# Kernel tuning notes

Hardware: AMD Instinct MI355X
Metric: run time of the kernel (lower is better)

## Reference

```python
import jax, jax.numpy as jnp
import numpy as np

B, S, H, V, T, L = 32, 128, 1024, 32000, 50, 3


def _ln(x, g, b, eps=1e-5):
    m = x.mean(-1, keepdims=True)
    v = ((x - m) ** 2).mean(-1, keepdims=True)
    return (x - m) / jnp.sqrt(v + eps) * g + b


def setup_inputs() -> dict:
    key = jax.random.key(0)
    ks = iter(jax.random.split(key, 48))
    r = lambda shape, s=0.02: jax.random.normal(next(ks), shape, jnp.float32) * s
    return dict(
        encoder_outputs=jax.random.normal(next(ks), (B, S, H), jnp.float32),
        h0=jax.random.normal(next(ks), (L, B, H), jnp.float32),
        c0=jax.random.normal(next(ks), (L, B, H), jnp.float32),
        valid_src_len=jax.random.randint(next(ks), (B,), 1, S + 1),
        target=jax.random.randint(next(ks), (B, T), 0, V),
        embedding=r((V, H), 1.0),
        Wa=r((H, H)), ba=jnp.zeros((H,)),
        Ua=r((H, H)), ub=jnp.zeros((H,)),
        Va=r((1, H)), vb=jnp.zeros((1,)),
        temperature=jnp.ones((1,)),
        Wih0=r((4 * H, 2 * H)), Whh0=r((4 * H, H)), bih0=jnp.zeros((4 * H,)), bhh0=jnp.zeros((4 * H,)),
        Wih1=r((4 * H, H)), Whh1=r((4 * H, H)), bih1=jnp.zeros((4 * H,)), bhh1=jnp.zeros((4 * H,)),
        Wih2=r((4 * H, H)), Whh2=r((4 * H, H)), bih2=jnp.zeros((4 * H,)), bhh2=jnp.zeros((4 * H,)),
        fc_w=r((V, H)), fc_b=jnp.zeros((V,)),
        eng=jnp.ones((H,)), enb=jnp.zeros((H,)),
        cng=jnp.ones((H,)), cnb=jnp.zeros((H,)),
        ong=jnp.ones((H,)), onb=jnp.zeros((H,)),
    )


def _decode(encoder_outputs, h0, c0, valid_src_len, target, p):
    mask = jnp.arange(S)[None, :] < valid_src_len[:, None]           # (B,S)
    Ukeys = encoder_outputs @ p['Ua'].T + p['ub']                    # (B,S,H) precomputed Ua(keys)
    Wih = (p['Wih0'], p['Wih1'], p['Wih2'])
    Whh = (p['Whh0'], p['Whh1'], p['Whh2'])
    bih = (p['bih0'], p['bih1'], p['bih2'])
    bhh = (p['bhh0'], p['bhh1'], p['bhh2'])
    # teacher forcing: token at step t is start_token (0) for t=0, else target[:, t-1]
    tokens = jnp.concatenate([jnp.zeros((B, 1), target.dtype), target[:, :-1]], 1).T  # (T,B)

    def step(carry, tok):
        h, c = carry                                                 # each (L,B,H)
        emb = _ln(p['embedding'][tok], p['eng'], p['enb'])           # (B,H); dropout omitted (eval)
        q = h[-1]                                                    # (B,H) query = top-layer h
        s = jnp.tanh((q @ p['Wa'].T + p['ba'])[:, None, :] + Ukeys)  # (B,S,H)
        scores = (jnp.einsum('bsh,h->bs', s, p['Va'][0]) + p['vb'][0]) / p['temperature'][0]
        scores = jnp.where(mask, scores, -1e9)
        w = jax.nn.softmax(scores, axis=-1)                          # (B,S)
        ctx = _ln(jnp.einsum('bs,bsh->bh', w, encoder_outputs), p['cng'], p['cnb'])
        x = jnp.concatenate([emb, ctx], axis=-1)                     # (B,2H)
        hs, cs = [], []
        for l in range(L):                                           # 3 stacked LSTM layers
            g = x @ Wih[l].T + bih[l] + h[l] @ Whh[l].T + bhh[l]
            i_, f_, g_, o_ = jnp.split(g, 4, axis=-1)                # torch gate order i,f,g,o
            cl = jax.nn.sigmoid(f_) * c[l] + jax.nn.sigmoid(i_) * jnp.tanh(g_)
            hl = jax.nn.sigmoid(o_) * jnp.tanh(cl)
            hs.append(hl); cs.append(cl); x = hl
        out = _ln(x, p['ong'], p['onb'])
        logits = out @ p['fc_w'].T + p['fc_b']                       # (B,V)
        return (jnp.stack(hs), jnp.stack(cs)), (logits, w)

    (hT, cT), (logits, attn) = jax.lax.scan(step, (h0, c0), tokens)
    return logits.transpose(1, 0, 2), hT, cT, attn.transpose(1, 0, 2)


def reference(encoder_outputs, h0, c0, valid_src_len, target, embedding, Wa, ba, Ua, ub, Va, vb,
              temperature, Wih0, Whh0, bih0, bhh0, Wih1, Whh1, bih1, bhh1, Wih2, Whh2, bih2, bhh2,
              fc_w, fc_b, eng, enb, cng, cnb, ong, onb):
    p = dict(embedding=embedding, Wa=Wa, ba=ba, Ua=Ua, ub=ub, Va=Va, vb=vb, temperature=temperature,
             Wih0=Wih0, Whh0=Whh0, bih0=bih0, bhh0=bhh0, Wih1=Wih1, Whh1=Whh1, bih1=bih1, bhh1=bhh1,
             Wih2=Wih2, Whh2=Whh2, bih2=bih2, bhh2=bhh2, fc_w=fc_w, fc_b=fc_b,
             eng=eng, enb=enb, cng=cng, cnb=cnb, ong=ong, onb=onb)
    logits, hT, cT, attn = _decode(encoder_outputs, h0, c0, valid_src_len, target, p)
    return logits, (hT, cT), attn
```

## Files before the change

kernel.cpp:

```cpp
#include <hip/hip_runtime.h>
#include <math.h>

#define DEV_INLINE __device__ __forceinline__

constexpr int B = 32, S = 128, H = 1024, V = 32000, T = 50, L = 3;
constexpr int H2 = 2 * H, H4 = 4 * H;
constexpr int BH = B * H;
constexpr int MTOT = T * B;

constexpr size_t HT_OFF   = (size_t)B * T * V;
constexpr size_t CT_OFF   = HT_OFF + (size_t)L * B * H;
constexpr size_t ATTN_OFF = CT_OFF + (size_t)L * B * H;

constexpr size_t WS_UKEYS = 0;
constexpr size_t WS_EMBBF = WS_UKEYS + (size_t)B * S * H;
constexpr size_t WS_H2ALL = WS_EMBBF + (size_t)T * BH / 2;
constexpr size_t WS_H     = WS_H2ALL + (size_t)T * BH;
constexpr size_t WS_C     = WS_H + (size_t)L * BH;
constexpr size_t WS_QWA   = WS_C + (size_t)L * BH;
constexpr size_t WS_SCO   = WS_QWA + (size_t)BH;
constexpr size_t WS_GAT   = WS_SCO + (size_t)B * S;
constexpr size_t WS_HBF   = WS_GAT + (size_t)B * H4;
constexpr size_t WS_XCBF  = WS_HBF + (size_t)2 * L * BH / 2;
constexpr size_t WS_OLALL = WS_XCBF + (size_t)B * H2 / 2;
constexpr size_t WS_WBF   = WS_OLALL + (size_t)T * BH / 2;

constexpr size_t OW_WA   = 0;
constexpr size_t OW_WIH0 = OW_WA   + (size_t)H * H;
constexpr size_t OW_WHH0 = OW_WIH0 + (size_t)H4 * H2;
constexpr size_t OW_WIH1 = OW_WHH0 + (size_t)H4 * H;
constexpr size_t OW_WHH1 = OW_WIH1 + (size_t)H4 * H;
constexpr size_t OW_WIH2 = OW_WHH1 + (size_t)H4 * H;
constexpr size_t OW_WHH2 = OW_WIH2 + (size_t)H4 * H;
constexpr size_t OW_FCW  = OW_WHH2 + (size_t)H4 * H;
constexpr size_t OW_END  = OW_FCW  + (size_t)V * H;
constexpr size_t NEED_WS_BYTES = WS_WBF * 4 + OW_END * 2;

typedef __attribute__((ext_vector_type(8))) short short8;
typedef __attribute__((ext_vector_type(4))) float f32x4;
typedef __attribute__((ext_vector_type(4))) unsigned short u16x4;

DEV_INLINE float sigmoidf_(float x) { return 1.f / (1.f + expf(-x)); }

DEV_INLINE unsigned short bf16u(float f) {
  union { float f; unsigned u; } v; v.f = f;
  unsigned r = v.u + 0x7fffu + ((v.u >> 16) & 1u);
  return (unsigned short)(r >> 16);
}

DEV_INLINE float wave_sum(float v) {
#pragma unroll
  for (int o = 32; o; o >>= 1) v += __shfl_xor(v, o, 64);
  return v;
}

DEV_INLINE float blk_sum256(float v, float* buf) {
  v = wave_sum(v);
  __syncthreads();
  if ((threadIdx.x & 63) == 0) buf[threadIdx.x >> 6] = v;
  __syncthreads();
  return buf[0] + buf[1] + buf[2] + buf[3];
}

__global__ void k_init(const float* __restrict__ h0, const float* __restrict__ c0,
                       float* __restrict__ hst, float* __restrict__ cst,
                       unsigned short* __restrict__ hbf) {
  int idx = blockIdx.x * 256 + threadIdx.x;
  if (idx < L * BH) { hst[idx] = h0[idx]; hbf[idx] = bf16u(h0[idx]); }
  else cst[idx - L * BH] = c0[idx - L * BH];
}

__global__ void k_fin(const float* __restrict__ hst, const float* __restrict__ h2src,
                      const float* __restrict__ cst, float* __restrict__ out) {
  int idx = blockIdx.x * 256 + threadIdx.x;
  if (idx < 2 * BH) out[HT_OFF + idx] = hst[idx];
  else if (idx < 3 * BH) out[HT_OFF + idx] = h2src[idx - 2 * BH];
  else out[HT_OFF + idx] = cst[idx - 3 * BH];
}

constexpr int NCVT = 8;
struct CvtArgs { const float* src[NCVT]; unsigned short* dst[NCVT]; };
constexpr int CV_N4[NCVT] = {
  H * H / 4, H4 * H2 / 4, H4 * H / 4, H4 * H / 4, H4 * H / 4,
  H4 * H / 4, H4 * H / 4, V * H / 4};
__global__ void k_cvt_all(CvtArgs a) {
  int cum[NCVT + 1]; cum[0] = 0;
#pragma unroll
  for (int r = 0; r < NCVT; ++r) cum[r + 1] = cum[r] + CV_N4[r];
  const int total = cum[NCVT];
  int i = blockIdx.x * 256 + threadIdx.x;
  const int stride = gridDim.x * 256;
  for (; i < total; i += stride) {
    int r = 0;
#pragma unroll
    for (int q = 0; q < NCVT; ++q) r += (i >= cum[q + 1]) ? 1 : 0;
    int off = i - cum[r];
    f32x4 v = *(const f32x4*)(a.src[r] + (size_t)off * 4);
    u16x4 o;
    o[0] = bf16u(v[0]); o[1] = bf16u(v[1]); o[2] = bf16u(v[2]); o[3] = bf16u(v[3]);
    *(u16x4*)(a.dst[r] + (size_t)off * 4) = o;
  }
}

__global__ __launch_bounds__(512) void k_ukeys_mfma(
    const float* __restrict__ X, const float* __restrict__ W,
    const float* __restrict__ bias, float* __restrict__ C) {
  __shared__ unsigned short As[128][72];
  __shared__ unsigned short Bs[128][72];
  const int tid = threadIdx.x, lane = tid & 63, wid = tid >> 6;
  const int wm = wid >> 2, wn = wid & 3;
  const int n0 = blockIdx.x * 128, m0 = blockIdx.y * 128;
  const int fr = lane & 15, kg = lane >> 4;
  f32x4 acc[4][2];
#pragma unroll
  for (int i = 0; i < 4; ++i)
#pragma unroll
    for (int j = 0; j < 2; ++j) acc[i][j] = {0.f, 0.f, 0.f, 0.f};
  for (int k0 = 0; k0 < H; k0 += 64) {
    __syncthreads();
#pragma unroll
    for (int r = 0; r < 4; ++r) {
      int i = tid + 512 * r;
      int row = i >> 4, c4 = (i & 15) * 4;
      f32x4 v = *(const f32x4*)(X + (size_t)(m0 + row) * H + k0 + c4);
      u16x4 o;
      o[0] = bf16u(v[0]); o[1] = bf16u(v[1]); o[2] = bf16u(v[2]); o[3] = bf16u(v[3]);
      *(u16x4*)&As[row][c4] = o;
    }
#pragma unroll
    for (int r = 0; r < 4; ++r) {
      int i = tid + 512 * r;
      int row = i >> 4, c4 = (i & 15) * 4;
      f32x4 v = *(const f32x4*)(W + (size_t)(n0 + row) * H + k0 + c4);
      u16x4 o;
      o[0] = bf16u(v[0]); o[1] = bf16u(v[1]); o[2] = bf16u(v[2]); o[3] = bf16u(v[3]);
      *(u16x4*)&Bs[row][c4] = o;
    }
    __syncthreads();
#pragma unroll
    for (int kk = 0; kk < 64; kk += 32) {
      short8 av[4], bv[2];
#pragma unroll
      for (int fm = 0; fm < 4; ++fm)
        av[fm] = *(const short8*)&As[wm * 64 + fm * 16 + fr][kk + kg * 8];
#pragma unroll
      for (int fn = 0; fn < 2; ++fn)
        bv[fn] = *(const short8*)&Bs[wn * 32 + fn * 16 + fr][kk + kg * 8];
#pragma unroll
      for (int fm = 0; fm < 4; ++fm)
#pragma unroll
        for (int fn = 0; fn < 2; ++fn)
          acc[fm][fn] = __builtin_amdgcn_mfma_f32_16x16x32_bf16(av[fm], bv[fn],
                                                                acc[fm][fn], 0, 0, 0);
    }
  }
#pragma unroll
  for (int fm = 0; fm < 4; ++fm)
#pragma unroll
    for (int fn = 0; fn < 2; ++fn)
#pragma unroll
      for (int r = 0; r < 4; ++r) {
        int m = m0 + wm * 64 + fm * 16 + kg * 4 + r;
        int n = n0 + wn * 32 + fn * 16 + fr;
        C[(size_t)m * H + n] = acc[fm][fn][r] + bias[n];
      }
}

__global__ __launch_bounds__(256) void k_gemm_nt(
    const float* __restrict__ A, const float* __restrict__ Bw,
    const float* __restrict__ bias, float* __restrict__ C, int N, int K) {
  __shared__ float As[16][132];
  __shared__ float Bs[16][68];
  const int i0 = blockIdx.y * 128, j0 = blockIdx.x * 64;
  const int ty = threadIdx.x >> 4, tx = threadIdx.x & 15;
  float acc[8][4] = {};
  for (int k0 = 0; k0 < K; k0 += 16) {
#pragma unroll
    for (int r = 0; r < 8; ++r) {
      int i = threadIdx.x + 256 * r;
      int mm = i >> 4, kk = i & 15;
      As[kk][mm] = A[(size_t)(i0 + mm) * K + k0 + kk];
    }
#pragma unroll
    for (int r = 0; r < 4; ++r) {
      int i = threadIdx.x + 256 * r;
      int nn = i >> 4, kk = i & 15;
      Bs[kk][nn] = Bw[(size_t)(j0 + nn) * K + k0 + kk];
    }
    __syncthreads();
#pragma unroll
    for (int kk = 0; kk < 16; ++kk) {
      float a[8], bb[4];
#pragma unroll
      for (int i = 0; i < 8; ++i) a[i] = As[kk][ty * 8 + i];
#pragma unroll
      for (int j = 0; j < 4; ++j) bb[j] = Bs[kk][tx * 4 + j];
#pragma unroll
      for (int i = 0; i < 8; ++i)
#pragma unroll
        for (int j = 0; j < 4; ++j) acc[i][j] = fmaf(a[i], bb[j], acc[i][j]);
    }
    __syncthreads();
  }
#pragma unroll
  for (int i = 0; i < 8; ++i) {
    size_t row = (size_t)(i0 + ty * 8 + i) * N;
#pragma unroll
    for (int j = 0; j < 4; ++j) {
      int col = j0 + tx * 4 + j;
      C[row + col] = acc[i][j] + bias[col];
    }
  }
}

__global__ void k_embln(const float* __restrict__ table, const int* __restrict__ target,
                        const float* __restrict__ g, const float* __restrict__ bta,
                        unsigned short* __restrict__ out) {
  __shared__ float rbuf[4];
  int idx = blockIdx.x;
  int t = idx >> 5, b = idx & 31;
  int tok = (t == 0) ? 0 : target[b * T + (t - 1)];
  const float* e = table + (size_t)tok * H;
  int tid = threadIdx.x;
  float x[4];
#pragma unroll
  for (int r = 0; r < 4; ++r) x[r] = e[r * 256 + tid];
  float m = blk_sum256(x[0] + x[1] + x[2] + x[3], rbuf) * (1.f / H);
  float vs = 0.f;
#pragma unroll
  for (int r = 0; r < 4; ++r) { float d = x[r] - m; vs += d * d; }
  float var = blk_sum256(vs, rbuf) * (1.f / H);
  float rstd = rsqrtf(var + 1e-5f);
  unsigned short* o = out + (size_t)idx * H;
#pragma unroll
  for (int r = 0; r < 4; ++r) {
    int h = r * 256 + tid;
    o[h] = bf16u((x[r] - m) * rstd * g[h] + bta[h]);
  }
}

__global__ void k_scores(const float* __restrict__ qwa, const float* __restrict__ ukeys,
                         const float* __restrict__ va, const float* __restrict__ vb,
                         const float* __restrict__ temp, const int* __restrict__ vlen,
                         float* __restrict__ sco) {
  int lane = threadIdx.x & 63, wid = threadIdx.x >> 6;
  int idx = blockIdx.x * 4 + wid;
  int b = idx >> 7, s = idx & 127;
  const float* uk = ukeys + (size_t)idx * H;
  const float* q = qwa + (size_t)b * H;
  float a = 0.f;
#pragma unroll
  for (int i = 0; i < 16; ++i) {
    int k = i * 64 + lane;
    a = fmaf(va[k], tanhf(q[k] + uk[k]), a);
  }
  a = wave_sum(a);
  if (lane == 0) {
    float val = (a + vb[0]) / temp[0];
    if (s >= vlen[b]) val = -1e9f;
    sco[idx] = val;
  }
}

__global__ void k_smctx(const float* __restrict__ sco, const float* __restrict__ enc,
                        const unsigned short* __restrict__ embt, const float* __restrict__ g,
                        const float* __restrict__ bta, unsigned short* __restrict__ xbf,
                        float* __restrict__ attn, int t) {
  __shared__ float sw[S];
  __shared__ float rbuf[4];
  int b = blockIdx.x, tid = threadIdx.x;
  if (tid < 64) {
    float v0 = sco[b * S + tid], v1 = sco[b * S + 64 + tid];
    float m = fmaxf(v0, v1);
#pragma unroll
    for (int o = 32; o; o >>= 1) m = fmaxf(m, __shfl_xor(m, o, 64));
    float e0 = expf(v0 - m), e1 = expf(v1 - m);
    float ssum = wave_sum(e0 + e1);
    float inv = 1.f / ssum;
    sw[tid] = e0 * inv;
    sw[64 + tid] = e1 * inv;
  }
  __syncthreads();
  if (tid < S) attn[((size_t)b * T + t) * S + tid] = sw[tid];
  float v[4] = {0.f, 0.f, 0.f, 0.f};
  for (int s2 = 0; s2 < S; ++s2) {
    float wv = sw[s2];
    const float* er = enc + ((size_t)b * S + s2) * H;
#pragma unroll
    for (int r = 0; r < 4; ++r) v[r] = fmaf(wv, er[r * 256 + tid], v[r]);
  }
  float m = blk_sum256(v[0] + v[1] + v[2] + v[3], rbuf) * (1.f / H);
  float vs = 0.f;
#pragma unroll
  for (int r = 0; r < 4; ++r) { float d = v[r] - m; vs += d * d; }
  float var = blk_sum256(vs, rbuf) * (1.f / H);
  float rstd = rsqrtf(var + 1e-5f);
  unsigned short* xr = xbf + (size_t)b * H2;
#pragma unroll
  for (int r = 0; r < 4; ++r) {
    int h = r * 256 + tid;
    xr[H + h] = bf16u((v[r] - m) * rstd * g[h] + bta[h]);
    xr[h] = embt[(size_t)b * H + h];
  }
}

__global__ __launch_bounds__(256) void k_skinny_bf(
    const unsigned short* __restrict__ x, const unsigned short* __restrict__ Wb, int K,
    const float* __restrict__ bias, float* __restrict__ out, int obstride) {
  __shared__ float red[4][32][16];
  const int lane = threadIdx.x & 63, wid = threadIdx.x >> 6;
  const int jb = blockIdx.x * 16;
  const int jl = lane & 15, kg = lane >> 4;
  f32x4 acc0 = {0.f, 0.f, 0.f, 0.f}, acc1 = {0.f, 0.f, 0.f, 0.f};
  const int per = (K >> 5) >> 2;
  const int send = (wid + 1) * per;
  for (int s = wid * per; s < send; ++s) {
    const int ke = s * 32 + kg * 8;
    short8 bw = *(const short8*)(Wb + (size_t)(jb + jl) * K + ke);
    short8 a0 = *(const short8*)(x + (size_t)jl * K + ke);
    short8 a1 = *(const short8*)(x + (size_t)(16 + jl) * K + ke);
    acc0 = __builtin_amdgcn_mfma_f32_16x16x32_bf16(a0, bw, acc0, 0, 0, 0);
    acc1 = __builtin_amdgcn_mfma_f32_16x16x32_bf16(a1, bw, acc1, 0, 0, 0);
  }
#pragma unroll
  for (int r = 0; r < 4; ++r) {
    red[wid][kg * 4 + r][jl] = acc0[r];
    red[wid][16 + kg * 4 + r][jl] = acc1[r];
  }
  __syncthreads();
  const int tid = threadIdx.x;
#pragma unroll
  for (int u = 0; u < 2; ++u) {
    int oi = tid * 2 + u;
    int m = oi >> 4, j = oi & 15;
    float v = red[0][m][j] + red[1][m][j] + red[2][m][j] + red[3][m][j];
    int jg = jb + j;
    out[(size_t)m * obstride + jg] = v + bias[jg];
  }
}

__global__ __launch_bounds__(256) void k_gates4(
    const unsigned short* __restrict__ x1, int K1,
    const unsigned short* __restrict__ x2, int K2,
    const unsigned short* __restrict__ W1, const unsigned short* __restrict__ W2,
    const float* __restrict__ bih, const float* __restrict__ bhh,
    float* __restrict__ cl, float* __restrict__ hl, unsigned short* __restrict__ hbfw) {
  __shared__ float red[4][32][17];
  const int lane = threadIdx.x & 63, wid = threadIdx.x >> 6;
  const int jb = blockIdx.x * 4;
  const int fr = lane & 15, kg = lane >> 4;
  const int wrow = (fr >> 2) * H + jb + (fr & 3);
  f32x4 acc0 = {0.f, 0.f, 0.f, 0.f}, acc1 = {0.f, 0.f, 0.f, 0.f};
  const int s1 = K1 >> 5, s2 = K2 >> 5;
  const int per = (s1 + s2) >> 2;
  const int sbeg = wid * per, send = sbeg + per;
  const int e1 = send < s1 ? send : s1;
#pragma unroll 4
  for (int s = sbeg; s < e1; ++s) {
    const int ke = s * 32 + kg * 8;
    short8 bw = *(const short8*)(W1 + (size_t)wrow * K1 + ke);
    short8 a0 = *(const short8*)(x1 + (size_t)fr * K1 + ke);
    short8 a1 = *(const short8*)(x1 + (size_t)(16 + fr) * K1 + ke);
    acc0 = __builtin_amdgcn_mfma_f32_16x16x32_bf16(a0, bw, acc0, 0, 0, 0);
    acc1 = __builtin_amdgcn_mfma_f32_16x16x32_bf16(a1, bw, acc1, 0, 0, 0);
  }
  const int b2 = sbeg > s1 ? sbeg : s1;
#pragma unroll 4
  for (int s = b2; s < send; ++s) {
    const int ke = (s - s1) * 32 + kg * 8;
    short8 bw = *(const short8*)(W2 + (size_t)wrow * K2 + ke);
    short8 a0 = *(const short8*)(x2 + (size_t)fr * K2 + ke);
    short8 a1 = *(const short8*)(x2 + (size_t)(16 + fr) * K2 + ke);
    acc0 = __builtin_amdgcn_mfma_f32_16x16x32_bf16(a0, bw, acc0, 0, 0, 0);
    acc1 = __builtin_amdgcn_mfma_f32_16x16x32_bf16(a1, bw, acc1, 0, 0, 0);
  }
#pragma unroll
  for (int r = 0; r < 4; ++r) {
    red[wid][kg * 4 + r][fr] = acc0[r];
    red[wid][16 + kg * 4 + r][fr] = acc1[r];
  }
  __syncthreads();
  const int tid = threadIdx.x;
  if (tid < 128) {
    int m = tid >> 2, jj = tid & 3, kcol = jb + jj;
    float gate[4];
#pragma unroll
    for (int g = 0; g < 4; ++g) {
      int f = g * 4 + jj;
      gate[g] = red[0][m][f] + red[1][m][f] + red[2][m][f] + red[3][m][f]
              + bih[g * H + kcol] + bhh[g * H + kcol];
    }
    int idx = m * H + kcol;
    float cn = sigmoidf_(gate[1]) * cl[idx] + sigmoidf_(gate[0]) * tanhf(gate[2]);
    float hn = sigmoidf_(gate[3]) * tanhf(cn);
    cl[idx] = cn;
    hl[idx] = hn;
    hbfw[idx] = bf16u(hn);
  }
}

__global__ void k_ln_all(const float* __restrict__ h2all, const float* __restrict__ g,
                         const float* __restrict__ bta, unsigned short* __restrict__ olbf) {
  __shared__ float rbuf[4];
  int row = blockIdx.x, tid = threadIdx.x;
  const float* hr = h2all + (size_t)row * H;
  float hv[4];
#pragma unroll
  for (int r = 0; r < 4; ++r) hv[r] = hr[r * 256 + tid];
  float m = blk_sum256(hv[0] + hv[1] + hv[2] + hv[3], rbuf) * (1.f / H);
  float vs = 0.f;
#pragma unroll
  for (int r = 0; r < 4; ++r) { float d = hv[r] - m; vs += d * d; }
  float var = blk_sum256(vs, rbuf) * (1.f / H);
  float rstd = rsqrtf(var + 1e-5f);
  unsigned short* o = olbf + (size_t)row * H;
#pragma unroll
  for (int r = 0; r < 4; ++r) {
    int k = r * 256 + tid;
    o[k] = bf16u((hv[r] - m) * rstd * g[k] + bta[k]);
  }
}

__global__ __launch_bounds__(512) void k_logits(
    const unsigned short* __restrict__ X, const unsigned short* __restrict__ Wb,
    const float* __restrict__ bias, float* __restrict__ out) {
  __shared__ unsigned short As[128][72];
  __shared__ unsigned short Bs[128][72];
  const int tid = threadIdx.x, lane = tid & 63, wid = tid >> 6;
  const int wm = wid >> 2, wn = wid & 3;
  const int n0 = blockIdx.x * 128, m0 = blockIdx.y * 128;
  const int fr = lane & 15, kg = lane >> 4;
  f32x4 acc[4][2];
#pragma unroll
  for (int i = 0; i < 4; ++i)
#pragma unroll
    for (int j = 0; j < 2; ++j) acc[i][j] = {0.f, 0.f, 0.f, 0.f};
  const short8 zero8 = {0, 0, 0, 0, 0, 0, 0, 0};
  for (int k0 = 0; k0 < H; k0 += 64) {
    __syncthreads();
#pragma unroll
    for (int r = 0; r < 2; ++r) {
      int i = tid + 512 * r, row = i >> 3, c8 = (i & 7) * 8;
      int gm = m0 + row;
      short8 v = (gm < MTOT) ? *(const short8*)(X + (size_t)gm * H + k0 + c8) : zero8;
      *(short8*)&As[row][c8] = v;
    }
#pragma unroll
    for (int r = 0; r < 2; ++r) {
      int i = tid + 512 * r, row = i >> 3, c8 = (i & 7) * 8;
      *(short8*)&Bs[row][c8] = *(const short8*)(Wb + (size_t)(n0 + row) * H + k0 + c8);
    }
    __syncthreads();
#pragma unroll
    for (int kk = 0; kk < 64; kk += 32) {
      short8 av[4], bv[2];
#pragma unroll
      for (int fm = 0; fm < 4; ++fm)
        av[fm] = *(const short8*)&As[wm * 64 + fm * 16 + fr][kk + kg * 8];
#pragma unroll
      for (int fn = 0; fn < 2; ++fn)
        bv[fn] = *(const short8*)&Bs[wn * 32 + fn * 16 + fr][kk + kg * 8];
#pragma unroll
      for (int fm = 0; fm < 4; ++fm)
#pragma unroll
        for (int fn = 0; fn < 2; ++fn)
          acc[fm][fn] = __builtin_amdgcn_mfma_f32_16x16x32_bf16(av[fm], bv[fn],
                                                                acc[fm][fn], 0, 0, 0);
    }
  }
#pragma unroll
  for (int fm = 0; fm < 4; ++fm)
#pragma unroll
    for (int fn = 0; fn < 2; ++fn)
#pragma unroll
      for (int r = 0; r < 4; ++r) {
        int m = m0 + wm * 64 + fm * 16 + kg * 4 + r;
        if (m < MTOT) {
          int n = n0 + wn * 32 + fn * 16 + fr;
          int b = m & 31, t = m >> 5;
          out[((size_t)b * T + t) * V + n] = acc[fm][fn][r] + bias[n];
        }
      }
}

__global__ __launch_bounds__(256) void k_mfma_skinny(
    const unsigned short* __restrict__ x1, const float* __restrict__ W1, int K1,
    const unsigned short* __restrict__ x2, const float* __restrict__ W2, int K2,
    const float* __restrict__ b1, const float* __restrict__ b2,
    float* __restrict__ out, int obstride) {
  __shared__ float red[4][32][16];
  const int lane = threadIdx.x & 63, wid = threadIdx.x >> 6;
  const int jb = blockIdx.x * 16;
  const int jl = lane & 15, kg = lane >> 4;
  f32x4 acc0 = {0.f, 0.f, 0.f, 0.f}, acc1 = {0.f, 0.f, 0.f, 0.f};
  const int s1 = K1 >> 5, s2 = K2 >> 5;
  const int per = (s1 + s2) >> 2;
  const int send = (wid + 1) * per;
  for (int s = wid * per; s < send; ++s) {
    const unsigned short* x; const float* W; int K, k0;
    if (s < s1) { x = x1; W = W1; K = K1; k0 = s * 32; }
    else       { x = x2; W = W2; K = K2; k0 = (s - s1) * 32; }
    const int ke = k0 + kg * 8;
    const float* wp = W + (size_t)(jb + jl) * K + ke;
    f32x4 w0 = *(const f32x4*)wp;
    f32x4 w1 = *(const f32x4*)(wp + 4);
    short8 bw;
    bw[0] = (short)bf16u(w0[0]); bw[1] = (short)bf16u(w0[1]);
    bw[2] = (short)bf16u(w0[2]); bw[3] = (short)bf16u(w0[3]);
    bw[4] = (short)bf16u(w1[0]); bw[5] = (short)bf16u(w1[1]);
    bw[6] = (short)bf16u(w1[2]); bw[7] = (short)bf16u(w1[3]);
    short8 a0 = *(const short8*)(x + (size_t)jl * K + ke);
    short8 a1 = *(const short8*)(x + (size_t)(16 + jl) * K + ke);
    acc0 = __builtin_amdgcn_mfma_f32_16x16x32_bf16(a0, bw, acc0, 0, 0, 0);
    acc1 = __builtin_amdgcn_mfma_f32_16x16x32_bf16(a1, bw, acc1, 0, 0, 0);
  }
#pragma unroll
  for (int r = 0; r < 4; ++r) {
    red[wid][kg * 4 + r][jl] = acc0[r];
    red[wid][16 + kg * 4 + r][jl] = acc1[r];
  }
  __syncthreads();
  const int tid = threadIdx.x;
#pragma unroll
  for (int u = 0; u < 2; ++u) {
    int oi = tid * 2 + u;
    int m = oi >> 4, j = oi & 15;
    float v = red[0][m][j] + red[1][m][j] + red[2][m][j] + red[3][m][j];
    int jg = jb + j;
    v += (b1 ? b1[jg] : 0.f) + (b2 ? b2[jg] : 0.f);
    out[(size_t)m * obstride + jg] = v;
  }
}

__global__ void k_cell(const float* __restrict__ gat, float* __restrict__ cl,
                       float* __restrict__ hl, unsigned short* __restrict__ hbf) {
  int idx = blockIdx.x * 256 + threadIdx.x;
  int b = idx >> 10, k = idx & 1023;
  const float* gb = gat + (size_t)b * H4;
  float i_ = gb[k], f_ = gb[H + k], g_ = gb[2 * H + k], o_ = gb[3 * H + k];
  float cn = sigmoidf_(f_) * cl[idx] + sigmoidf_(i_) * tanhf(g_);
  float hn = sigmoidf_(o_) * tanhf(cn);
  cl[idx] = cn;
  hl[idx] = hn;
  hbf[idx] = bf16u(hn);
}

__global__ void k_cell2ln(const float* __restrict__ gat, float* __restrict__ cl,
                          float* __restrict__ hl, const float* __restrict__ g,
                          const float* __restrict__ bta, unsigned short* __restrict__ olbf,
                          unsigned short* __restrict__ hbf) {
  __shared__ float rbuf[4];
  int b = blockIdx.x, tid = threadIdx.x;
  const float* gb = gat + (size_t)b * H4;
  float hv[4];
#pragma unroll
  for (int r = 0; r < 4; ++r) {
    int k = r * 256 + tid;
    float i_ = gb[k], f_ = gb[H + k], g_ = gb[2 * H + k], o_ = gb[3 * H + k];
    float cn = sigmoidf_(f_) * cl[b * H + k] + sigmoidf_(i_) * tanhf(g_);
    float hn = sigmoidf_(o_) * tanhf(cn);
    cl[b * H + k] = cn;
    hl[b * H + k] = hn;
    hbf[b * H + k] = bf16u(hn);
    hv[r] = hn;
  }
  float m = blk_sum256(hv[0] + hv[1] + hv[2] + hv[3], rbuf) * (1.f / H);
  float vs = 0.f;
#pragma unroll
  for (int r = 0; r < 4; ++r) { float d = hv[r] - m; vs += d * d; }
  float var = blk_sum256(vs, rbuf) * (1.f / H);
  float rstd = rsqrtf(var + 1e-5f);
#pragma unroll
  for (int r = 0; r < 4; ++r) {
    int k = r * 256 + tid;
    olbf[b * H + k] = bf16u((hv[r] - m) * rstd * g[k] + bta[k]);
  }
}

extern "C" void kernel_launch(void* const* d_in, const int* in_sizes, int n_in,
                              void* d_out, int out_size, void* d_ws, size_t ws_size,
                              hipStream_t stream) {
  (void)in_sizes; (void)n_in; (void)out_size;
  const float* enc = (const float*)d_in[0];
  const float* h0 = (const float*)d_in[1];
  const float* c0 = (const float*)d_in[2];
  const int* vlen = (const int*)d_in[3];
  const int* target = (const int*)d_in[4];
  const float* emb_table = (const float*)d_in[5];
  const float* Wa = (const float*)d_in[6];
  const float* ba = (const float*)d_in[7];
  const float* Ua = (const float*)d_in[8];
  const float* ub = (const float*)d_in[9];
  const float* Va = (const float*)d_in[10];
  const float* vb = (const float*)d_in[11];
  const float* temp = (const float*)d_in[12];
  const float* Wih[3] = {(const float*)d_in[13], (const float*)d_in[17], (const float*)d_in[21]};
  const float* Whh[3] = {(const float*)d_in[14], (const float*)d_in[18], (const float*)d_in[22]};
  const float* bih[3] = {(const float*)d_in[15], (const float*)d_in[19], (const float*)d_in[23]};
  const float* bhh[3] = {(const float*)d_in[16], (const float*)d_in[20], (const float*)d_in[24]};
  const float* fcw = (const float*)d_in[25];
  const float* fcb = (const float*)d_in[26];
  const float* eng = (const float*)d_in[27];
  const float* enb = (const float*)d_in[28];
  const float* cng = (const float*)d_in[29];
  const float* cnb = (const float*)d_in[30];
  const float* ong = (const float*)d_in[31];
  const float* onb = (const float*)d_in[32];

  float* ws = (float*)d_ws;
  float* ukeys = ws + WS_UKEYS;
  unsigned short* embbf = (unsigned short*)(ws + WS_EMBBF);
  float* h2all = ws + WS_H2ALL;
  float* hst = ws + WS_H;
  float* cst = ws + WS_C;
  float* qwa = ws + WS_QWA;
  float* sco = ws + WS_SCO;
  float* gat = ws + WS_GAT;
  unsigned short* hbf = (unsigned short*)(ws + WS_HBF);
  unsigned short* xcbf = (unsigned short*)(ws + WS_XCBF);
  unsigned short* olall = (unsigned short*)(ws + WS_OLALL);
  unsigned short* wbf = (unsigned short*)(ws + WS_WBF);
  float* out = (float*)d_out;

  const bool big = ws_size >= NEED_WS_BYTES;

  k_init<<<768, 256, 0, stream>>>(h0, c0, hst, cst, hbf);
  k_embln<<<T * B, 256, 0, stream>>>(emb_table, target, eng, enb, embbf);

  if (big) {
    k_ukeys_mfma<<<dim3(H / 128, (B * S) / 128), 512, 0, stream>>>(enc, Ua, ub, ukeys);

    CvtArgs ca;
    ca.src[0] = Wa;      ca.dst[0] = wbf + OW_WA;
    ca.src[1] = Wih[0];  ca.dst[1] = wbf + OW_WIH0;
    ca.src[2] = Whh[0];  ca.dst[2] = wbf + OW_WHH0;
    ca.src[3] = Wih[1];  ca.dst[3] = wbf + OW_WIH1;
    ca.src[4] = Whh[1];  ca.dst[4] = wbf + OW_WHH1;
    ca.src[5] = Wih[2];  ca.dst[5] = wbf + OW_WIH2;
    ca.src[6] = Whh[2];  ca.dst[6] = wbf + OW_WHH2;
    ca.src[7] = fcw;     ca.dst[7] = wbf + OW_FCW;
    k_cvt_all<<<2048, 256, 0, stream>>>(ca);

    for (int t = 0; t < T; ++t) {
      const unsigned short* rb = hbf + (size_t)(t & 1) * (L * BH);
      unsigned short* wb = hbf + (size_t)((t + 1) & 1) * (L * BH);
      k_skinny_bf<<<H / 16, 256, 0, stream>>>(rb + 2 * BH, wbf + OW_WA, H, ba, qwa, H);
      k_scores<<<(B * S) / 4, 256, 0, stream>>>(qwa, ukeys, Va, vb, temp, vlen, sco);
      k_smctx<<<B, 256, 0, stream>>>(sco, enc, embbf + (size_t)t * BH, cng, cnb, xcbf,
                                     out + ATTN_OFF, t);
      k_gates4<<<H / 4, 256, 0, stream>>>(xcbf, H2, rb, H,
                                          wbf + OW_WIH0, wbf + OW_WHH0,
                                          bih[0], bhh[0], cst, hst, wb);
      k_gates4<<<H / 4, 256, 0, stream>>>(wb, H, rb + BH, H,
                                          wbf + OW_WIH1, wbf + OW_WHH1,
                                          bih[1], bhh[1], cst + BH, hst + BH, wb + BH);
      k_gates4<<<H / 4, 256, 0, stream>>>(wb + BH, H, rb + 2 * BH, H,
                                          wbf + OW_WIH2, wbf + OW_WHH2,
                                          bih[2], bhh[2], cst + 2 * BH,
                                          h2all + (size_t)t * BH, wb + 2 * BH);
    }
    k_ln_all<<<T * B, 256, 0, stream>>>(h2all, ong, onb, olall);
    k_logits<<<dim3(V / 128, (MTOT + 127) / 128), 512, 0, stream>>>(olall, wbf + OW_FCW,
                                                                    fcb, out);
    k_fin<<<768, 256, 0, stream>>>(hst, h2all + (size_t)(T - 1) * BH, cst, out);
  } else {
    k_gemm_nt<<<dim3(H / 64, (B * S) / 128), 256, 0, stream>>>(enc, Ua, ub, ukeys, H, H);
    for (int t = 0; t < T; ++t) {
      k_mfma_skinny<<<H / 16, 256, 0, stream>>>(hbf + 2 * BH, Wa, H, nullptr, nullptr, 0,
                                                ba, nullptr, qwa, H);
      k_scores<<<(B * S) / 4, 256, 0, stream>>>(qwa, ukeys, Va, vb, temp, vlen, sco);
      k_smctx<<<B, 256, 0, stream>>>(sco, enc, embbf + (size_t)t * BH, cng, cnb, xcbf,
                                     out + ATTN_OFF, t);
      k_mfma_skinny<<<H4 / 16, 256, 0, stream>>>(xcbf, Wih[0], H2, hbf, Whh[0], H,
                                                 bih[0], bhh[0], gat, H4);
      k_cell<<<BH / 256, 256, 0, stream>>>(gat, cst, hst, hbf);
      k_mfma_skinny<<<H4 / 16, 256, 0, stream>>>(hbf, Wih[1], H, hbf + BH, Whh[1], H,
                                                 bih[1], bhh[1], gat, H4);
      k_cell<<<BH / 256, 256, 0, stream>>>(gat, cst + BH, hst + BH, hbf + BH);
      k_mfma_skinny<<<H4 / 16, 256, 0, stream>>>(hbf + BH, Wih[2], H, hbf + 2 * BH, Whh[2], H,
                                                 bih[2], bhh[2], gat, H4);
      k_cell2ln<<<B, 256, 0, stream>>>(gat, cst + 2 * BH, hst + 2 * BH, ong, onb,
                                       olall + (size_t)t * BH, hbf + 2 * BH);
      k_mfma_skinny<<<V / 16, 256, 0, stream>>>(olall + (size_t)t * BH, fcw, H,
                                                nullptr, nullptr, 0,
                                                fcb, nullptr, out + (size_t)t * V, T * V);
    }
    k_fin<<<768, 256, 0, stream>>>(hst, hst + 2 * BH, cst, out);
  }
}
```

Baseline: 3.256 ms.

## Fuse attention scores, softmax and context into one kernel; convert fc weights in GEMM

Replaces the separate scores and softmax/context kernels with a single 1024-thread kernel per batch row. It keeps query and Va in registers, computes scores with a fast exp-based tanh, then does the masked softmax, weighted context, layernorm and concat write in one launch. The separate fp32-to-bf16 pre-conversion of the large fc weight matrix is removed, and the logits GEMM now loads fp32 weights and converts them while filling shared memory. This cuts per-step launches and the 32000x1024 conversion pass, at the cost of twice the weight bytes read in the GEMM and a slightly less accurate tanh.

After: 4.037 ms. +24.0%, slower.

```diff
diff --git a/kernel.cpp b/kernel.cpp
--- a/kernel.cpp
+++ b/kernel.cpp
@@ -32,8 +32,7 @@
 constexpr size_t OW_WHH1 = OW_WIH1 + (size_t)H4 * H;
 constexpr size_t OW_WIH2 = OW_WHH1 + (size_t)H4 * H;
 constexpr size_t OW_WHH2 = OW_WIH2 + (size_t)H4 * H;
-constexpr size_t OW_FCW  = OW_WHH2 + (size_t)H4 * H;
-constexpr size_t OW_END  = OW_FCW  + (size_t)V * H;
+constexpr size_t OW_END  = OW_WHH2 + (size_t)H4 * H;
 constexpr size_t NEED_WS_BYTES = WS_WBF * 4 + OW_END * 2;
 
 typedef __attribute__((ext_vector_type(8))) short short8;
@@ -41,6 +40,11 @@
 typedef __attribute__((ext_vector_type(4))) unsigned short u16x4;
 
 DEV_INLINE float sigmoidf_(float x) { return 1.f / (1.f + expf(-x)); }
+
+DEV_INLINE float ftanh(float x) {
+  float e = __expf(2.f * x);
+  return 1.f - 2.f / (e + 1.f);
+}
 
 DEV_INLINE unsigned short bf16u(float f) {
   union { float f; unsigned u; } v; v.f = f;
@@ -60,6 +64,17 @@
   if ((threadIdx.x & 63) == 0) buf[threadIdx.x >> 6] = v;
   __syncthreads();
   return buf[0] + buf[1] + buf[2] + buf[3];
+}
+
+DEV_INLINE float blk_sum1024(float v, float* buf) {
+  v = wave_sum(v);
+  __syncthreads();
+  if ((threadIdx.x & 63) == 0) buf[threadIdx.x >> 6] = v;
+  __syncthreads();
+  float s = 0.f;
+#pragma unroll
+  for (int i = 0; i < 16; ++i) s += buf[i];
+  return s;
 }
 
 __global__ void k_init(const float* __restrict__ h0, const float* __restrict__ c0,
@@ -78,11 +93,11 @@
   else out[HT_OFF + idx] = cst[idx - 3 * BH];
 }
 
-constexpr int NCVT = 8;
+constexpr int NCVT = 7;
 struct CvtArgs { const float* src[NCVT]; unsigned short* dst[NCVT]; };
 constexpr int CV_N4[NCVT] = {
   H * H / 4, H4 * H2 / 4, H4 * H / 4, H4 * H / 4, H4 * H / 4,
-  H4 * H / 4, H4 * H / 4, V * H / 4};
+  H4 * H / 4, H4 * H / 4};
 __global__ void k_cvt_all(CvtArgs a) {
   int cum[NCVT + 1]; cum[0] = 0;
 #pragma unroll
@@ -237,6 +252,69 @@
     int h = r * 256 + tid;
     o[h] = bf16u((x[r] - m) * rstd * g[h] + bta[h]);
   }
+}
+
+__global__ __launch_bounds__(1024) void k_att(
+    const float* __restrict__ qwa, const float* __restrict__ ukeys,
+    const float* __restrict__ enc, const unsigned short* __restrict__ embt,
+    const float* __restrict__ va, const float* __restrict__ vb,
+    const float* __restrict__ temp, const int* __restrict__ vlen,
+    const float* __restrict__ g, const float* __restrict__ bta,
+    unsigned short* __restrict__ xbf, float* __restrict__ attn, int t) {
+  __shared__ float sco_s[S];
+  __shared__ float sw[S];
+  __shared__ float rbuf[16];
+  const int b = blockIdx.x, tid = threadIdx.x;
+  const int lane = tid & 63, w = tid >> 6;
+  float qR[16], vaR[16];
+  {
+    const float* qp = qwa + (size_t)b * H + lane * 16;
+    const float* vp = va + lane * 16;
+#pragma unroll
+    for (int j = 0; j < 16; ++j) { qR[j] = qp[j]; vaR[j] = vp[j]; }
+  }
+#pragma unroll
+  for (int i = 0; i < 8; ++i) {
+    int s = w * 8 + i;
+    const float* up = ukeys + ((size_t)(b * S + s)) * H + lane * 16;
+    float a = 0.f;
+#pragma unroll
+    for (int j = 0; j < 16; ++j) a = fmaf(vaR[j], ftanh(qR[j] + up[j]), a);
+    a = wave_sum(a);
+    if (lane == 0) sco_s[s] = a;
+  }
+  __syncthreads();
+  if (tid < 64) {
+    float vbv = vb[0], tmp = temp[0];
+    int vl = vlen[b];
+    float v0 = (sco_s[tid] + vbv) / tmp;
+    float v1 = (sco_s[64 + tid] + vbv) / tmp;
+    if (tid >= vl) v0 = -1e9f;
+    if (64 + tid >= vl) v1 = -1e9f;
+    float m = fmaxf(v0, v1);
+#pragma unroll
+    for (int o = 32; o; o >>= 1) m = fmaxf(m, __shfl_xor(m, o, 64));
+    float e0 = expf(v0 - m), e1 = expf(v1 - m);
+    float ssum = wave_sum(e0 + e1);
+    float inv = 1.f / ssum;
+    sw[tid] = e0 * inv;
+    sw[64 + tid] = e1 * inv;
+  }
+  __syncthreads();
+  if (tid < S) attn[((size_t)b * T + t) * S + tid] = sw[tid];
+  float v = 0.f;
+  {
+    const float* ep = enc + (size_t)b * S * H + tid;
+#pragma unroll 4
+    for (int s2 = 0; s2 < S; ++s2) v = fmaf(sw[s2], ep[(size_t)s2 * H], v);
+  }
+  float m = blk_sum1024(v, rbuf) * (1.f / H);
+  float d = v - m;
+  float var = blk_sum1024(d * d, rbuf) * (1.f / H);
+  float rstd = rsqrtf(var + 1e-5f);
+  unsigned short* xr = xbf + (size_t)b * H2;
+  xr[H + tid] = bf16u(d * rstd * g[tid] + bta[tid]);
+  xr[tid] = embt[(size_t)b * H + tid];
 }
 
 __global__ void k_scores(const float* __restrict__ qwa, const float* __restrict__ ukeys,
@@ -422,7 +500,7 @@
 }
 
 __global__ __launch_bounds__(512) void k_logits(
-    const unsigned short* __restrict__ X, const unsigned short* __restrict__ Wb,
+    const unsigned short* __restrict__ X, const float* __restrict__ W,
     const float* __restrict__ bias, float* __restrict__ out) {
   __shared__ unsigned short As[128][72];
   __shared__ unsigned short Bs[128][72];
@@ -446,9 +524,13 @@
       *(short8*)&As[row][c8] = v;
     }
 #pragma unroll
-    for (int r = 0; r < 2; ++r) {
-      int i = tid + 512 * r, row = i >> 3, c8 = (i & 7) * 8;
-      *(short8*)&Bs[row][c8] = *(const short8*)(Wb + (size_t)(n0 + row) * H + k0 + c8);
+    for (int r = 0; r < 4; ++r) {
+      int i = tid + 512 * r;
+      int row = i >> 4, c4 = (i & 15) * 4;
+      f32x4 v = *(const f32x4*)(W + (size_t)(n0 + row) * H + k0 + c4);
+      u16x4 o;
+      o[0] = bf16u(v[0]); o[1] = bf16u(v[1]); o[2] = bf16u(v[2]); o[3] = bf16u(v[3]);
+      *(u16x4*)&Bs[row][c4] = o;
     }
     __syncthreads();
 #pragma unroll
@@ -638,16 +720,15 @@
     ca.src[4] = Whh[1];  ca.dst[4] = wbf + OW_WHH1;
     ca.src[5] = Wih[2];  ca.dst[5] = wbf + OW_WIH2;
     ca.src[6] = Whh[2];  ca.dst[6] = wbf + OW_WHH2;
-    ca.src[7] = fcw;     ca.dst[7] = wbf + OW_FCW;
     k_cvt_all<<<2048, 256, 0, stream>>>(ca);
 
     for (int t = 0; t < T; ++t) {
       const unsigned short* rb = hbf + (size_t)(t & 1) * (L * BH);
       unsigned short* wb = hbf + (size_t)((t + 1) & 1) * (L * BH);
       k_skinny_bf<<<H / 16, 256, 0, stream>>>(rb + 2 * BH, wbf + OW_WA, H, ba, qwa, H);
-      k_scores<<<(B * S) / 4, 256, 0, stream>>>(qwa, ukeys, Va, vb, temp, vlen, sco);
-      k_smctx<<<B, 256, 0, stream>>>(sco, enc, embbf + (size_t)t * BH, cng, cnb, xcbf,
-                                     out + ATTN_OFF, t);
+      k_att<<<B, 1024, 0, stream>>>(qwa, ukeys, enc, embbf + (size_t)t * BH,
+                                    Va, vb, temp, vlen, cng, cnb, xcbf,
+                                    out + ATTN_OFF, t);
       k_gates4<<<H / 4, 256, 0, stream>>>(xcbf, H2, rb, H,
                                           wbf + OW_WIH0, wbf + OW_WHH0,
                                           bih[0], bhh[0], cst, hst, wb);
@@ -660,8 +741,7 @@
                                           h2all + (size_t)t * BH, wb + 2 * BH);
     }
     k_ln_all<<<T * B, 256, 0, stream>>>(h2all, ong, onb, olall);
-    k_logits<<<dim3(V / 128, (MTOT + 127) / 128), 512, 0, stream>>>(olall, wbf + OW_FCW,
-                                                                    fcb, out);
+    k_logits<<<dim3(V / 128, (MTOT + 127) / 128), 512, 0, stream>>>(olall, fcw, fcb, out);
     k_fin<<<768, 256, 0, stream>>>(hst, h2all + (size_t)(T - 1) * BH, cst, out);
   } else {
     k_gemm_nt<<<dim3(H / 64, (B * S) / 128), 256, 0, stream>>>(enc, Ua, ub, ukeys, H, H);
```
